# Kernel optimization log

Measured on AMD Instinct MI355X. Metric: run time of the kernel, lower is better.

The kernel has to match this reference:

```python
import jax, jax.numpy as jnp
import numpy as np
from jax import lax

B, H, W = 4096, 15, 15
P, V = 16, 32
D = P + V            # 48
PCODE = 2380
NEMB = 2 * (PCODE + 1)  # 4762


def _conv(x, w, b=None, groups=1, pad='SAME'):
    # x: [B,C,H,W], w: [O, I/groups, kh, kw] (torch OIHW layout)
    y = lax.conv_general_dilated(
        x, w, window_strides=(1, 1), padding=pad,
        dimension_numbers=('NCHW', 'OIHW', 'NCHW'),
        feature_group_count=groups)
    if b is not None:
        y = y + b[None, :, None, None]
    return y


def setup_inputs() -> dict:
    key = jax.random.key(0)
    ks = jax.random.split(key, 18)
    f = lambda k, shape: (jax.random.normal(k, shape, jnp.float32) * 0.05)
    inp = {
        'emb': f(ks[0], (NEMB, D)),
        'conv_w': f(ks[1], (D, 1, 3, 3)),      # depthwise, groups=D
        'conv_b': f(ks[2], (D,)),
        'ppw_w': f(ks[3], (P, P, 1, 1)),
        'ppw_b': f(ks[4], (P,)),
        'pdw_w': f(ks[5], (P, 1, 3, 3)),       # depthwise, groups=P
        'pdw_b': f(ks[6], (P,)),
        'pf_w': f(ks[7], (1, P, 1, 1)),        # final policy conv, no bias
        'vpw_w': f(ks[8], (V, V, 1, 1)),
        'vpw_b': f(ks[9], (V,)),
        'vl1_w': f(ks[10], (V, V)),
        'vl1_b': f(ks[11], (V,)),
        'vl2_w': f(ks[12], (V, V)),
        'vl2_b': f(ks[13], (V,)),
        'vf_w': f(ks[14], (3, V)),
        'vf_b': f(ks[15], (3,)),
        'sparse_feature_input': jax.random.randint(ks[16], (B, 12, H, W), 0, PCODE, jnp.int32),
        'board_input': jax.random.randint(ks[17], (B, 2, H, W), 0, 2, jnp.int32),
    }
    return inp


def reference(emb, conv_w, conv_b, ppw_w, ppw_b, pdw_w, pdw_b, pf_w,
              vpw_w, vpw_b, vl1_w, vl1_b, vl2_w, vl2_b, vf_w, vf_b,
              sparse_feature_input, board_input):
    relu = jax.nn.relu
    # --- PatternCodeEmbedding ---
    pcode = sparse_feature_input[:, 10:12]                     # [B,2,H,W]
    pcode = jnp.where(board_input > 0, PCODE, pcode)
    pcode = pcode + jnp.array([0, PCODE + 1], jnp.int32)[None, :, None, None]
    feat = emb[pcode].sum(axis=1)                              # [B,H,W,D]
    feat = jnp.transpose(feat, (0, 3, 1, 2))                   # [B,D,H,W]
    # --- trunk depthwise conv ---
    feat = relu(_conv(feat, conv_w, conv_b, groups=D))
    # --- policy head ---
    pol = feat[:, :P]
    pol = relu(_conv(pol, ppw_w, ppw_b))
    pol = relu(_conv(pol, pdw_w, pdw_b, groups=P))
    pol = _conv(pol, pf_w)                                     # [B,1,H,W]
    # --- value head ---
    val = feat[:, P:]
    val = relu(_conv(val, vpw_w, vpw_b))
    val = jnp.mean(val, axis=(2, 3))                           # [B,V]
    val = relu(val @ vl1_w.T + vl1_b)
    val = relu(val @ vl2_w.T + vl2_b)
    val = val @ vf_w.T + vf_b                                  # [B,3]
    return val, pol
```

## Files before the change

kernel.cpp:

```cpp
#include <hip/hip_runtime.h>
#include <hip/hip_fp16.h>

typedef _Float16 half8  __attribute__((ext_vector_type(8)));
typedef _Float16 half4_t __attribute__((ext_vector_type(4)));
typedef _Float16 half2_t __attribute__((ext_vector_type(2)));
typedef float f32x4 __attribute__((ext_vector_type(4)));

namespace {
constexpr int NT = 256;
constexpr int NPIX = 225;
constexpr int PCODE_C = 2380;

constexpr int APITCH_Y  = 272;
constexpr int APITCH_CG = 4624;

constexpr int OFF_A     = 0;
constexpr int OFF_XLO   = 16224;
constexpr int OFF_XHI   = 27744;
constexpr int OFF_WCB   = 38544;
constexpr int OFF_WC    = 39264;
constexpr int OFF_SV    = 39264;
constexpr int OFF_H1    = 39392;
constexpr int OFF_H2    = 39520;
constexpr int OFF_WPD   = 40128;
constexpr int OFF_WPDB  = 40416;
constexpr int SMEM_BYTES = 40448;

constexpr int OFF_POLA  = 0;
}

__device__ __forceinline__ half2_t pkrtz(float a, float b) {
    return __builtin_bit_cast(half2_t, __builtin_amdgcn_cvt_pkrtz(a, b));
}
__device__ __forceinline__ void wave_fence() {
    asm volatile("s_waitcnt lgkmcnt(0)" ::: "memory");
}

__global__ __launch_bounds__(NT, 4) void patnet_kernel(
    const float* __restrict__ emb,
    const float* __restrict__ conv_w, const float* __restrict__ conv_b,
    const float* __restrict__ ppw_w,  const float* __restrict__ ppw_b,
    const float* __restrict__ pdw_w,  const float* __restrict__ pdw_b,
    const float* __restrict__ pf_w,
    const float* __restrict__ vpw_w,  const float* __restrict__ vpw_b,
    const float* __restrict__ vl1_w,  const float* __restrict__ vl1_b,
    const float* __restrict__ vl2_w,  const float* __restrict__ vl2_b,
    const float* __restrict__ vf_w,   const float* __restrict__ vf_b,
    const int* __restrict__ sparse,   const int* __restrict__ board,
    float* __restrict__ out, int batch)
{
    __shared__ __align__(16) unsigned char smem[SMEM_BYTES];
    const int tid  = threadIdx.x;
    const int b    = blockIdx.x;
    const int lane = tid & 63;
    const int wave = tid >> 6;

    int c0 = 0, c1 = 0;
    if (tid < NPIX) {
        int s10 = sparse[b * 2700 + 10 * NPIX + tid];
        int s11 = sparse[b * 2700 + 11 * NPIX + tid];
        int b0  = board[b * 450 + tid];
        int b1  = board[b * 450 + NPIX + tid];
        c0 = (b0 > 0) ? PCODE_C : s10;
        c1 = ((b1 > 0) ? PCODE_C : s11) + (PCODE_C + 1);
    }

    {
        _Float16* Wc   = (_Float16*)(smem + OFF_WC);
        _Float16* Wcb  = (_Float16*)(smem + OFF_WCB);
        _Float16* Wpd  = (_Float16*)(smem + OFF_WPD);
        _Float16* Wpdb = (_Float16*)(smem + OFF_WPDB);
        for (int i = tid; i < 432; i += NT) {
            int cg = i / 72, rem = i - cg * 72;
            int t = rem >> 3, j = rem & 7;
            Wc[i] = (_Float16)conv_w[(cg * 8 + j) * 9 + t];
        }
        for (int i = tid; i < 48; i += NT) Wcb[i] = (_Float16)conv_b[i];
        for (int i = tid; i < 144; i += NT) {
            int cg = i / 72, rem = i - cg * 72;
            int t = rem >> 3, j = rem & 7;
            Wpd[i] = (_Float16)pdw_w[(cg * 8 + j) * 9 + t];
        }
        for (int i = tid; i < 16; i += NT) Wpdb[i] = (_Float16)pdw_b[i];
        for (int i = tid; i < 384; i += NT) {
            int cg = i >> 6, j = i & 63;
            int row, col;
            if (j < 17)      { row = 0;  col = j; }
            else if (j < 34) { row = 16; col = j - 17; }
            else { int k = j - 34; row = 1 + (k >> 1); col = (k & 1) * 16; }
            *(half8*)(smem + OFF_A + cg * APITCH_CG + row * APITCH_Y + col * 16) = (half8)(_Float16)0.f;
        }
    }

    if (tid < NPIX) {
        const float* e0 = emb + c0 * 48;
        const float* e1 = emb + c1 * 48;
        int y = tid / 15, x = tid - y * 15;
        unsigned char* abase = smem + OFF_A + (y + 1) * APITCH_Y + (x + 1) * 16;
        #pragma unroll
        for (int g = 0; g < 6; g++) {
            f32x4 x0 = *(const f32x4*)(e0 + g * 8);
            f32x4 x1 = *(const f32x4*)(e0 + g * 8 + 4);
            f32x4 y0 = *(const f32x4*)(e1 + g * 8);
            f32x4 y1 = *(const f32x4*)(e1 + g * 8 + 4);
            f32x4 s0 = x0 + y0, s1 = x1 + y1;
            half2_t q0 = pkrtz(s0.x, s0.y), q1 = pkrtz(s0.z, s0.w);
            half2_t q2 = pkrtz(s1.x, s1.y), q3 = pkrtz(s1.z, s1.w);
            half8 hv = {q0[0], q0[1], q1[0], q1[1], q2[0], q2[1], q3[0], q3[1]};
            *(half8*)(abase + g * APITCH_CG) = hv;
        }
    }
    __syncthreads();

    auto do_strip = [&](int t, int cgbase, int xbase) {
        int cgl = t / 45, rem = t - cgl * 45;
        int y = rem / 3, s = rem - y * 3;
        int xs = s * 5;
        int cg = cgbase + cgl;
        const unsigned char* wb = smem + OFF_WC + cg * 144;
        half8 wv[9];
        #pragma unroll
        for (int i = 0; i < 9; i++) wv[i] = *(const half8*)(wb + i * 16);
        half8 bias = *(const half8*)(smem + OFF_WCB + cg * 16);
        half8 acc[5] = {bias, bias, bias, bias, bias};
        const unsigned char* ab = smem + OFF_A + cg * APITCH_CG + y * APITCH_Y + xs * 16;
        #pragma unroll
        for (int c = 0; c < 7; c++) {
            half8 v0 = *(const half8*)(ab + c * 16);
            half8 v1 = *(const half8*)(ab + APITCH_Y + c * 16);
            half8 v2 = *(const half8*)(ab + 2 * APITCH_Y + c * 16);
            #pragma unroll
            for (int o = 0; o < 5; o++) {
                int kx = c - o;
                if (kx >= 0 && kx <= 2) {
                    acc[o] = __builtin_elementwise_fma(v0, wv[kx],     acc[o]);
                    acc[o] = __builtin_elementwise_fma(v1, wv[3 + kx], acc[o]);
                    acc[o] = __builtin_elementwise_fma(v2, wv[6 + kx], acc[o]);
                }
            }
        }
        unsigned char* xw = smem + xbase + (y * 15 + xs) * 48 + cgl * 16;
        #pragma unroll
        for (int o = 0; o < 5; o++)
            *(half8*)(xw + o * 48) = __builtin_elementwise_max(acc[o], (half8)(_Float16)0.f);
    };
    if (tid < 135) do_strip(tid, 3, OFF_XHI);
    __syncthreads();
    if (tid < 135) do_strip(tid, 0, OFF_XLO);

    const int n = lane & 15, q = lane >> 4;
    const int cgp = lane & 1;
    half8 af_p;
    {
        const float* wp = ppw_w + n * 16 + (q & 1) * 8;
        f32x4 w0 = *(const f32x4*)wp, w1 = *(const f32x4*)(wp + 4);
        half8 t = {(_Float16)w0.x, (_Float16)w0.y, (_Float16)w0.z, (_Float16)w0.w,
                   (_Float16)w1.x, (_Float16)w1.y, (_Float16)w1.z, (_Float16)w1.w};
        af_p = (q < 2) ? t : (half8)(_Float16)0.f;
    }
    f32x4 pb = *(const f32x4*)(ppw_b + q * 4);
    half2_t pf0 = pkrtz(pf_w[cgp * 8 + 0], pf_w[cgp * 8 + 1]);
    half2_t pf1 = pkrtz(pf_w[cgp * 8 + 2], pf_w[cgp * 8 + 3]);
    half2_t pf2 = pkrtz(pf_w[cgp * 8 + 4], pf_w[cgp * 8 + 5]);
    half2_t pf3 = pkrtz(pf_w[cgp * 8 + 6], pf_w[cgp * 8 + 7]);
    half8 af0, af1;
    {
        const float* wp = vpw_w + n * 32 + q * 8;
        f32x4 w0 = *(const f32x4*)wp, w1 = *(const f32x4*)(wp + 4);
        af0 = half8{(_Float16)w0.x, (_Float16)w0.y, (_Float16)w0.z, (_Float16)w0.w,
                    (_Float16)w1.x, (_Float16)w1.y, (_Float16)w1.z, (_Float16)w1.w};
        const float* wp2 = vpw_w + (16 + n) * 32 + q * 8;
        f32x4 v0 = *(const f32x4*)wp2, v1 = *(const f32x4*)(wp2 + 4);
        af1 = half8{(_Float16)v0.x, (_Float16)v0.y, (_Float16)v0.z, (_Float16)v0.w,
                    (_Float16)v1.x, (_Float16)v1.y, (_Float16)v1.z, (_Float16)v1.w};
    }
    f32x4 vb0 = *(const f32x4*)(vpw_b + q * 4);
    f32x4 vb1 = *(const f32x4*)(vpw_b + 16 + q * 4);
    __syncthreads();

    if (wave < 3) {
        #pragma unroll
        for (int i0 = 0; i0 < 2; i0++) {
            int i = i0 * 64 + lane;
            int cg = i >> 6, j = i & 63;
            int row, col;
            if (j < 17)      { row = 0;  col = j; }
            else if (j < 34) { row = 16; col = j - 17; }
            else { int k = j - 34; row = 1 + (k >> 1); col = (k & 1) * 16; }
            *(half8*)(smem + OFF_POLA + cg * APITCH_CG + row * APITCH_Y + col * 16) = (half8)(_Float16)0.f;
        }
        half8 wvp[9];
        #pragma unroll
        for (int t = 0; t < 9; t++) wvp[t] = *(const half8*)(smem + OFF_WPD + cgp * 144 + t * 16);
        half8 biasp = *(const half8*)(smem + OFF_WPDB + cgp * 16);

        const int tlo = (wave == 0) ? 0 : ((wave == 1) ? 3 : 8);
        const int thi = (wave == 0) ? 6 : ((wave == 1) ? 11 : 15);
        const int cg3 = q >> 1;
        for (int t = tlo; t < thi; t++) {
            int p = t * 16 + n;
            half8 bf = *(const half8*)(smem + OFF_XLO + p * 48 + (q & 1) * 16);
            f32x4 d = __builtin_amdgcn_mfma_f32_16x16x32_f16(af_p, bf, (f32x4)(0.f), 0, 0, 0);
            if (p < NPIX) {
                int y = p / 15, x = p - y * 15;
                half2_t lo = pkrtz(fmaxf(d.x + pb.x, 0.f), fmaxf(d.y + pb.y, 0.f));
                half2_t hi = pkrtz(fmaxf(d.z + pb.z, 0.f), fmaxf(d.w + pb.w, 0.f));
                half4_t hv = {lo[0], lo[1], hi[0], hi[1]};
                *(half4_t*)(smem + OFF_POLA + cg3 * APITCH_CG + (y + 1) * APITCH_Y + (x + 1) * 16 + (q & 1) * 8) = hv;
            }
        }
        wave_fence();

        const int px0 = wave * 75;
        for (int i = 0; i < 3; i++) {
            int idx = i * 64 + lane;
            if (idx < 150) {
                int px = px0 + (idx >> 1);
                int y = px / 15, x = px - y * 15;
                const unsigned char* pbse = smem + OFF_POLA + cgp * APITCH_CG + y * APITCH_Y + x * 16;
                half8 acc = biasp;
                #pragma unroll
                for (int ky = 0; ky < 3; ky++) {
                    acc = __builtin_elementwise_fma(*(const half8*)(pbse + ky * APITCH_Y),      wvp[ky * 3 + 0], acc);
                    acc = __builtin_elementwise_fma(*(const half8*)(pbse + ky * APITCH_Y + 16), wvp[ky * 3 + 1], acc);
                    acc = __builtin_elementwise_fma(*(const half8*)(pbse + ky * APITCH_Y + 32), wvp[ky * 3 + 2], acc);
                }
                acc = __builtin_elementwise_max(acc, (half8)(_Float16)0.f);
                float part = 0.f;
                part = __builtin_amdgcn_fdot2(half2_t{acc[0], acc[1]}, pf0, part, false);
                part = __builtin_amdgcn_fdot2(half2_t{acc[2], acc[3]}, pf1, part, false);
                part = __builtin_amdgcn_fdot2(half2_t{acc[4], acc[5]}, pf2, part, false);
                part = __builtin_amdgcn_fdot2(half2_t{acc[6], acc[7]}, pf3, part, false);
                float tot = part + __shfl_xor(part, 1, 64);
                if (cgp == 0) out[3 * batch + b * NPIX + px] = tot;
            }
        }
    } else {
        const int xb = (q == 0) ? (OFF_XLO + 32) : (OFF_XHI + (q - 1) * 16);
        f32x4 a0 = {0.f, 0.f, 0.f, 0.f}, a1 = {0.f, 0.f, 0.f, 0.f};
        for (int t = 0; t < 15; t++) {
            int p = t * 16 + n;
            half8 bf = *(const half8*)(smem + xb + p * 48);
            f32x4 d0 = __builtin_amdgcn_mfma_f32_16x16x32_f16(af0, bf, (f32x4)(0.f), 0, 0, 0);
            f32x4 d1 = __builtin_amdgcn_mfma_f32_16x16x32_f16(af1, bf, (f32x4)(0.f), 0, 0, 0);
            if (p < NPIX) {
                #pragma unroll
                for (int r = 0; r < 4; r++) {
                    a0[r] += fmaxf(d0[r] + vb0[r], 0.f);
                    a1[r] += fmaxf(d1[r] + vb1[r], 0.f);
                }
            }
        }
        #pragma unroll
        for (int s = 1; s < 16; s <<= 1) {
            #pragma unroll
            for (int r = 0; r < 4; r++) {
                a0[r] += __shfl_xor(a0[r], s, 64);
                a1[r] += __shfl_xor(a1[r], s, 64);
            }
        }
        if (n == 0) {
            *(f32x4*)(smem + OFF_SV + q * 16)      = a0 * (1.f / 225.f);
            *(f32x4*)(smem + OFF_SV + 64 + q * 16) = a1 * (1.f / 225.f);
        }
        const int o = lane & 31;
        f32x4 wA[8];
        float b1v = vl1_b[o], b2v = vl2_b[o], b3v = 0.f;
        #pragma unroll
        for (int g = 0; g < 8; g++) wA[g] = *(const f32x4*)(vl1_w + o * 32 + g * 4);
        wave_fence();

        f32x4 wB[8];
        #pragma unroll
        for (int g = 0; g < 8; g++) wB[g] = *(const f32x4*)(vl2_w + o * 32 + g * 4);
        float acc1 = b1v;
        #pragma unroll
        for (int g = 0; g < 8; g++) {
            f32x4 sv = *(const f32x4*)(smem + OFF_SV + g * 16);
            acc1 += sv.x * wA[g].x + sv.y * wA[g].y + sv.z * wA[g].z + sv.w * wA[g].w;
        }
        acc1 = fmaxf(acc1, 0.f);
        if (lane < 32) *(float*)(smem + OFF_H1 + o * 4) = acc1;
        wave_fence();

        f32x4 wC[8];
        if (lane < 3) {
            b3v = vf_b[lane];
            #pragma unroll
            for (int g = 0; g < 8; g++) wC[g] = *(const f32x4*)(vf_w + lane * 32 + g * 4);
        }
        float acc2 = b2v;
        #pragma unroll
        for (int g = 0; g < 8; g++) {
            f32x4 hv = *(const f32x4*)(smem + OFF_H1 + g * 16);
            acc2 += hv.x * wB[g].x + hv.y * wB[g].y + hv.z * wB[g].z + hv.w * wB[g].w;
        }
        acc2 = fmaxf(acc2, 0.f);
        if (lane < 32) *(float*)(smem + OFF_H2 + o * 4) = acc2;
        wave_fence();

        if (lane < 3) {
            float acc3 = b3v;
            #pragma unroll
            for (int g = 0; g < 8; g++) {
                f32x4 hv = *(const f32x4*)(smem + OFF_H2 + g * 16);
                acc3 += hv.x * wC[g].x + hv.y * wC[g].y + hv.z * wC[g].z + hv.w * wC[g].w;
            }
            out[b * 3 + lane] = acc3;
        }
    }
}

extern "C" void kernel_launch(void* const* d_in, const int* in_sizes, int n_in,
                              void* d_out, int out_size, void* d_ws, size_t ws_size,
                              hipStream_t stream) {
    const float* emb    = (const float*)d_in[0];
    const float* conv_w = (const float*)d_in[1];
    const float* conv_b = (const float*)d_in[2];
    const float* ppw_w  = (const float*)d_in[3];
    const float* ppw_b  = (const float*)d_in[4];
    const float* pdw_w  = (const float*)d_in[5];
    const float* pdw_b  = (const float*)d_in[6];
    const float* pf_w   = (const float*)d_in[7];
    const float* vpw_w  = (const float*)d_in[8];
    const float* vpw_b  = (const float*)d_in[9];
    const float* vl1_w  = (const float*)d_in[10];
    const float* vl1_b  = (const float*)d_in[11];
    const float* vl2_w  = (const float*)d_in[12];
    const float* vl2_b  = (const float*)d_in[13];
    const float* vf_w   = (const float*)d_in[14];
    const float* vf_b   = (const float*)d_in[15];
    const int* sparse   = (const int*)d_in[16];
    const int* board    = (const int*)d_in[17];
    float* out = (float*)d_out;

    int batch = in_sizes[16] / 2700;
    patnet_kernel<<<batch, NT, 0, stream>>>(
        emb, conv_w, conv_b, ppw_w, ppw_b, pdw_w, pdw_b, pf_w,
        vpw_w, vpw_b, vl1_w, vl1_b, vl2_w, vl2_b, vf_w, vf_b,
        sparse, board, out, batch);
}
```

Measured before the change: 168.3 us.

## Shrink shared memory with unpadded rows, per-channel-group buffers and staged weight slots

Shared memory layout is reworked to drop the padded halo rows, using a shared zero row for vertical borders, and stores conv outputs in per-channel-group planar buffers instead of an interleaved layout. Conv weights are staged into two alternating slots just before each of three depthwise passes, which are now split into three phases of two channel groups. Launch bounds move from 4 to 5 blocks per CU. The goal is higher occupancy through a smaller LDS footprint, paid for with an extra barrier and pass plus pointer-selection logic for the borders.

Measured after the change: 186.6 us. 10.9% more time.

```diff
diff --git a/kernel.cpp b/kernel.cpp
--- a/kernel.cpp
+++ b/kernel.cpp
@@ -11,22 +11,25 @@
 constexpr int NPIX = 225;
 constexpr int PCODE_C = 2380;
 
-constexpr int APITCH_Y  = 272;
-constexpr int APITCH_CG = 4624;
+constexpr int AROW = 272;
+constexpr int ACG  = 4080;
 
 constexpr int OFF_A     = 0;
-constexpr int OFF_XLO   = 16224;
-constexpr int OFF_XHI   = 27744;
-constexpr int OFF_WCB   = 38544;
-constexpr int OFF_WC    = 39264;
-constexpr int OFF_SV    = 39264;
-constexpr int OFF_H1    = 39392;
-constexpr int OFF_H2    = 39520;
-constexpr int OFF_WPD   = 40128;
-constexpr int OFF_WPDB  = 40416;
-constexpr int SMEM_BYTES = 40448;
-
-constexpr int OFF_POLA  = 0;
+constexpr int OFF_POLA0 = 0;
+constexpr int OFF_POLA1 = 4080;
+constexpr int OFF_XC0   = 8160;
+constexpr int OFF_XC1   = 11760;
+constexpr int OFF_XC2   = 16320;
+constexpr int OFF_XC3   = 19920;
+constexpr int OFF_SV    = 23520;
+constexpr int OFF_H1    = 23648;
+constexpr int OFF_H2    = 23776;
+constexpr int OFF_XC4   = 24480;
+constexpr int OFF_XC5   = 28080;
+constexpr int OFF_ZROW  = 31680;
+constexpr int OFF_SLOTA = 31952;
+constexpr int OFF_SLOTB = 32272;
+constexpr int SMEM_BYTES = 32592;
 }
 
 __device__ __forceinline__ half2_t pkrtz(float a, float b) {
@@ -36,7 +39,7 @@
     asm volatile("s_waitcnt lgkmcnt(0)" ::: "memory");
 }
 
-__global__ __launch_bounds__(NT, 4) void patnet_kernel(
+__global__ __launch_bounds__(NT, 5) void patnet_kernel(
     const float* __restrict__ emb,
     const float* __restrict__ conv_w, const float* __restrict__ conv_b,
     const float* __restrict__ ppw_w,  const float* __restrict__ ppw_b,
@@ -65,30 +68,33 @@
         c1 = ((b1 > 0) ? PCODE_C : s11) + (PCODE_C + 1);
     }
 
-    {
-        _Float16* Wc   = (_Float16*)(smem + OFF_WC);
-        _Float16* Wcb  = (_Float16*)(smem + OFF_WCB);
-        _Float16* Wpd  = (_Float16*)(smem + OFF_WPD);
-        _Float16* Wpdb = (_Float16*)(smem + OFF_WPDB);
-        for (int i = tid; i < 432; i += NT) {
-            int cg = i / 72, rem = i - cg * 72;
-            int t = rem >> 3, j = rem & 7;
-            Wc[i] = (_Float16)conv_w[(cg * 8 + j) * 9 + t];
-        }
-        for (int i = tid; i < 48; i += NT) Wcb[i] = (_Float16)conv_b[i];
-        for (int i = tid; i < 144; i += NT) {
-            int cg = i / 72, rem = i - cg * 72;
-            int t = rem >> 3, j = rem & 7;
-            Wpd[i] = (_Float16)pdw_w[(cg * 8 + j) * 9 + t];
-        }
-        for (int i = tid; i < 16; i += NT) Wpdb[i] = (_Float16)pdw_b[i];
-        for (int i = tid; i < 384; i += NT) {
-            int cg = i >> 6, j = i & 63;
-            int row, col;
-            if (j < 17)      { row = 0;  col = j; }
-            else if (j < 34) { row = 16; col = j - 17; }
-            else { int k = j - 34; row = 1 + (k >> 1); col = (k & 1) * 16; }
-            *(half8*)(smem + OFF_A + cg * APITCH_CG + row * APITCH_Y + col * 16) = (half8)(_Float16)0.f;
+    auto stage_w = [&](int slotOff, const float* wsrc, const float* bsrc, int cgbase) {
+        int i = tid - 96;
+        if (i >= 0 && i < 160) {
+            int cgl = i / 80, r = i - cgl * 80;
+            _Float16 v;
+            if (r < 72) {
+                int t = r >> 3, j = r & 7;
+                v = (_Float16)wsrc[((cgbase + cgl) * 8 + j) * 9 + t];
+            } else {
+                v = (_Float16)bsrc[(cgbase + cgl) * 8 + (r - 72)];
+            }
+            ((_Float16*)(smem + slotOff))[i] = v;
+        }
+    };
+
+    stage_w(OFF_SLOTA, conv_w, conv_b, 4);
+    if (tid < 96) {
+        for (int i = tid; i < 197; i += 96) {
+            unsigned char* dst;
+            if (i < 180) {
+                int cg = i / 30, r = i - cg * 30;
+                int row = r >> 1, colB = (r & 1) * 256;
+                dst = smem + OFF_A + cg * ACG + row * AROW + colB;
+            } else {
+                dst = smem + OFF_ZROW + (i - 180) * 16;
+            }
+            *(half8*)dst = (half8)(_Float16)0.f;
         }
     }
 
@@ -96,7 +102,7 @@
         const float* e0 = emb + c0 * 48;
         const float* e1 = emb + c1 * 48;
         int y = tid / 15, x = tid - y * 15;
-        unsigned char* abase = smem + OFF_A + (y + 1) * APITCH_Y + (x + 1) * 16;
+        unsigned char* abase = smem + OFF_A + y * AROW + (x + 1) * 16;
         #pragma unroll
         for (int g = 0; g < 6; g++) {
             f32x4 x0 = *(const f32x4*)(e0 + g * 8);
@@ -107,28 +113,30 @@
             half2_t q0 = pkrtz(s0.x, s0.y), q1 = pkrtz(s0.z, s0.w);
             half2_t q2 = pkrtz(s1.x, s1.y), q3 = pkrtz(s1.z, s1.w);
             half8 hv = {q0[0], q0[1], q1[0], q1[1], q2[0], q2[1], q3[0], q3[1]};
-            *(half8*)(abase + g * APITCH_CG) = hv;
+            *(half8*)(abase + g * ACG) = hv;
         }
     }
     __syncthreads();
 
-    auto do_strip = [&](int t, int cgbase, int xbase) {
+    auto do_strip = [&](int t, int cgbase, int slotOff, int xBase) {
         int cgl = t / 45, rem = t - cgl * 45;
         int y = rem / 3, s = rem - y * 3;
-        int xs = s * 5;
-        int cg = cgbase + cgl;
-        const unsigned char* wb = smem + OFF_WC + cg * 144;
+        const unsigned char* wb = smem + slotOff + cgl * 160;
         half8 wv[9];
         #pragma unroll
         for (int i = 0; i < 9; i++) wv[i] = *(const half8*)(wb + i * 16);
-        half8 bias = *(const half8*)(smem + OFF_WCB + cg * 16);
+        half8 bias = *(const half8*)(wb + 144);
         half8 acc[5] = {bias, bias, bias, bias, bias};
-        const unsigned char* ab = smem + OFF_A + cg * APITCH_CG + y * APITCH_Y + xs * 16;
+        const unsigned char* abase = smem + OFF_A + (cgbase + cgl) * ACG;
+        const unsigned char* r0 = (y >= 1)  ? abase + (y - 1) * AROW : smem + OFF_ZROW;
+        const unsigned char* r1 = abase + y * AROW;
+        const unsigned char* r2 = (y <= 13) ? abase + (y + 1) * AROW : smem + OFF_ZROW;
+        int xo = s * 80;
         #pragma unroll
         for (int c = 0; c < 7; c++) {
-            half8 v0 = *(const half8*)(ab + c * 16);
-            half8 v1 = *(const half8*)(ab + APITCH_Y + c * 16);
-            half8 v2 = *(const half8*)(ab + 2 * APITCH_Y + c * 16);
+            half8 v0 = *(const half8*)(r0 + xo + c * 16);
+            half8 v1 = *(const half8*)(r1 + xo + c * 16);
+            half8 v2 = *(const half8*)(r2 + xo + c * 16);
             #pragma unroll
             for (int o = 0; o < 5; o++) {
                 int kx = c - o;
@@ -139,14 +147,20 @@
                 }
             }
         }
-        unsigned char* xw = smem + xbase + (y * 15 + xs) * 48 + cgl * 16;
+        unsigned char* xw = smem + xBase + cgl * 3600 + (y * 15 + s * 5) * 16;
         #pragma unroll
         for (int o = 0; o < 5; o++)
-            *(half8*)(xw + o * 48) = __builtin_elementwise_max(acc[o], (half8)(_Float16)0.f);
+            *(half8*)(xw + o * 16) = __builtin_elementwise_max(acc[o], (half8)(_Float16)0.f);
     };
-    if (tid < 135) do_strip(tid, 3, OFF_XHI);
+
+    if (tid < 90) do_strip(tid, 4, OFF_SLOTA, OFF_XC4);
+    stage_w(OFF_SLOTB, conv_w, conv_b, 2);
     __syncthreads();
-    if (tid < 135) do_strip(tid, 0, OFF_XLO);
+    if (tid < 90) do_strip(tid, 2, OFF_SLOTB, OFF_XC2);
+    stage_w(OFF_SLOTA, conv_w, conv_b, 0);
+    __syncthreads();
+    if (tid < 90) do_strip(tid, 0, OFF_SLOTA, OFF_XC0);
+    stage_w(OFF_SLOTB, pdw_w, pdw_b, 0);
 
     const int n = lane & 15, q = lane >> 4;
     const int cgp = lane & 1;
@@ -179,34 +193,31 @@
     __syncthreads();
 
     if (wave < 3) {
-        #pragma unroll
-        for (int i0 = 0; i0 < 2; i0++) {
-            int i = i0 * 64 + lane;
-            int cg = i >> 6, j = i & 63;
-            int row, col;
-            if (j < 17)      { row = 0;  col = j; }
-            else if (j < 34) { row = 16; col = j - 17; }
-            else { int k = j - 34; row = 1 + (k >> 1); col = (k & 1) * 16; }
-            *(half8*)(smem + OFF_POLA + cg * APITCH_CG + row * APITCH_Y + col * 16) = (half8)(_Float16)0.f;
+        if (lane < 60) {
+            int cg = lane / 30, r = lane - cg * 30;
+            int row = r >> 1, colB = (r & 1) * 256;
+            *(half8*)(smem + OFF_POLA0 + cg * ACG + row * AROW + colB) = (half8)(_Float16)0.f;
         }
         half8 wvp[9];
         #pragma unroll
-        for (int t = 0; t < 9; t++) wvp[t] = *(const half8*)(smem + OFF_WPD + cgp * 144 + t * 16);
-        half8 biasp = *(const half8*)(smem + OFF_WPDB + cgp * 16);
+        for (int t = 0; t < 9; t++) wvp[t] = *(const half8*)(smem + OFF_SLOTB + cgp * 160 + t * 16);
+        half8 biasp = *(const half8*)(smem + OFF_SLOTB + cgp * 160 + 144);
 
         const int tlo = (wave == 0) ? 0 : ((wave == 1) ? 3 : 8);
         const int thi = (wave == 0) ? 6 : ((wave == 1) ? 11 : 15);
         const int cg3 = q >> 1;
+        const int xbp = (q & 1) ? OFF_XC1 : OFF_XC0;
         for (int t = tlo; t < thi; t++) {
             int p = t * 16 + n;
-            half8 bf = *(const half8*)(smem + OFF_XLO + p * 48 + (q & 1) * 16);
+            int pc = (p > 224) ? 224 : p;
+            half8 bf = *(const half8*)(smem + xbp + pc * 16);
             f32x4 d = __builtin_amdgcn_mfma_f32_16x16x32_f16(af_p, bf, (f32x4)(0.f), 0, 0, 0);
             if (p < NPIX) {
                 int y = p / 15, x = p - y * 15;
                 half2_t lo = pkrtz(fmaxf(d.x + pb.x, 0.f), fmaxf(d.y + pb.y, 0.f));
                 half2_t hi = pkrtz(fmaxf(d.z + pb.z, 0.f), fmaxf(d.w + pb.w, 0.f));
                 half4_t hv = {lo[0], lo[1], hi[0], hi[1]};
-                *(half4_t*)(smem + OFF_POLA + cg3 * APITCH_CG + (y + 1) * APITCH_Y + (x + 1) * 16 + (q & 1) * 8) = hv;
+                *(half4_t*)(smem + OFF_POLA0 + cg3 * ACG + y * AROW + (x + 1) * 16 + (q & 1) * 8) = hv;
             }
         }
         wave_fence();
@@ -217,14 +228,21 @@
             if (idx < 150) {
                 int px = px0 + (idx >> 1);
                 int y = px / 15, x = px - y * 15;
-                const unsigned char* pbse = smem + OFF_POLA + cgp * APITCH_CG + y * APITCH_Y + x * 16;
+                const unsigned char* base = smem + OFF_POLA0 + cgp * ACG;
+                const unsigned char* pm = (y > 0)  ? base + (y - 1) * AROW : smem + OFF_ZROW;
+                const unsigned char* pz = base + y * AROW;
+                const unsigned char* pp = (y < 14) ? base + (y + 1) * AROW : smem + OFF_ZROW;
+                int xo = x * 16;
                 half8 acc = biasp;
-                #pragma unroll
-                for (int ky = 0; ky < 3; ky++) {
-                    acc = __builtin_elementwise_fma(*(const half8*)(pbse + ky * APITCH_Y),      wvp[ky * 3 + 0], acc);
-                    acc = __builtin_elementwise_fma(*(const half8*)(pbse + ky * APITCH_Y + 16), wvp[ky * 3 + 1], acc);
-                    acc = __builtin_elementwise_fma(*(const half8*)(pbse + ky * APITCH_Y + 32), wvp[ky * 3 + 2], acc);
-                }
+                acc = __builtin_elementwise_fma(*(const half8*)(pm + xo),      wvp[0], acc);
+                acc = __builtin_elementwise_fma(*(const half8*)(pm + xo + 16), wvp[1], acc);
+                acc = __builtin_elementwise_fma(*(const half8*)(pm + xo + 32), wvp[2], acc);
+                acc = __builtin_elementwise_fma(*(const half8*)(pz + xo),      wvp[3], acc);
+                acc = __builtin_elementwise_fma(*(const half8*)(pz + xo + 16), wvp[4], acc);
+                acc = __builtin_elementwise_fma(*(const half8*)(pz + xo + 32), wvp[5], acc);
+                acc = __builtin_elementwise_fma(*(const half8*)(pp + xo),      wvp[6], acc);
+                acc = __builtin_elementwise_fma(*(const half8*)(pp + xo + 16), wvp[7], acc);
+                acc = __builtin_elementwise_fma(*(const half8*)(pp + xo + 32), wvp[8], acc);
                 acc = __builtin_elementwise_max(acc, (half8)(_Float16)0.f);
                 float part = 0.f;
                 part = __builtin_amdgcn_fdot2(half2_t{acc[0], acc[1]}, pf0, part, false);
@@ -236,11 +254,12 @@
             }
         }
     } else {
-        const int xb = (q == 0) ? (OFF_XLO + 32) : (OFF_XHI + (q - 1) * 16);
+        const int xb = (q < 2) ? (OFF_XC2 + q * 3600) : (OFF_XC4 + (q - 2) * 3600);
         f32x4 a0 = {0.f, 0.f, 0.f, 0.f}, a1 = {0.f, 0.f, 0.f, 0.f};
         for (int t = 0; t < 15; t++) {
             int p = t * 16 + n;
-            half8 bf = *(const half8*)(smem + xb + p * 48);
+            int pc = (p > 224) ? 224 : p;
+            half8 bf = *(const half8*)(smem + xb + pc * 16);
             f32x4 d0 = __builtin_amdgcn_mfma_f32_16x16x32_f16(af0, bf, (f32x4)(0.f), 0, 0, 0);
             f32x4 d1 = __builtin_amdgcn_mfma_f32_16x16x32_f16(af1, bf, (f32x4)(0.f), 0, 0, 0);
             if (p < NPIX) {
```
